# Performance work log

Measured on AMD Instinct MI355X. Metric: run time of the kernel, lower is better.

## Reference

```python
import jax, jax.numpy as jnp
import numpy as np

V = 1000   # vocab_size
E = 1024   # encoder_output_dim
D = 512    # decoder_hidden_dim
A = 512    # attention_hidden_dim
T = 128    # token_embedding_size
B = 128    # batch
P = 196    # num_pix (14x14)
L = 257    # latex length -> 256 decode steps


def setup_inputs() -> dict:
    key = jax.random.key(0)
    ks = jax.random.split(key, 16)
    def p(k, shape, scale=0.05):
        return (jax.random.normal(k, shape, jnp.float32) * scale)
    return dict(
        features=jax.random.normal(ks[0], (B, P, E), jnp.float32),
        latexes=jax.random.randint(ks[1], (B, L), 0, V),
        emb=p(ks[2], (V, T)),
        Wenc=p(ks[3], (A, E)), benc=jnp.zeros((A,), jnp.float32),
        Wdec=p(ks[4], (A, D)), bdec=jnp.zeros((A,), jnp.float32),
        Wattn=p(ks[5], (1, A)), battn=jnp.zeros((1,), jnp.float32),
        W1ih=p(ks[6], (4 * D, E + T)), W1hh=p(ks[7], (4 * D, D)),
        b1ih=jnp.zeros((4 * D,), jnp.float32), b1hh=jnp.zeros((4 * D,), jnp.float32),
        W2ih=p(ks[8], (4 * D, D)), W2hh=p(ks[9], (4 * D, D)),
        b2ih=jnp.zeros((4 * D,), jnp.float32), b2hh=jnp.zeros((4 * D,), jnp.float32),
        Wh0=p(ks[10], (D, E)), bh0=jnp.zeros((D,), jnp.float32),
        Wc0=p(ks[11], (D, E)), bc0=jnp.zeros((D,), jnp.float32),
        Wg=p(ks[12], (E, D)), bg=jnp.zeros((E,), jnp.float32),
        Wf=p(ks[13], (V, D)), bf=jnp.zeros((V,), jnp.float32),
    )


def _lstm_cell(x, h, c, Wih, Whh, bih, bhh):
    # torch.nn.LSTMCell: gates order i, f, g, o
    g = x @ Wih.T + bih + h @ Whh.T + bhh
    i, f, gg, o = jnp.split(g, 4, axis=1)
    c_new = jax.nn.sigmoid(f) * c + jax.nn.sigmoid(i) * jnp.tanh(gg)
    h_new = jax.nn.sigmoid(o) * jnp.tanh(c_new)
    return h_new, c_new


def reference(features, latexes, emb, Wenc, benc, Wdec, bdec, Wattn, battn,
              W1ih, W1hh, b1ih, b1hh, W2ih, W2hh, b2ih, b2hh,
              Wh0, bh0, Wc0, bc0, Wg, bg, Wf, bf):
    seq_length = latexes.shape[1] - 1
    embeds = emb[latexes]                      # [B, L, T]
    mean_enc = features.mean(axis=1)           # [B, E]
    h1 = mean_enc @ Wh0.T + bh0
    c1 = mean_enc @ Wc0.T + bc0
    h2, c2 = h1, c1
    # encoder branch of attention is step-invariant; hoist out of the loop
    enc_t = features @ Wenc.T + benc           # [B, P, A]
    wa = Wattn[0]                              # [A]
    ba = battn[0]

    def step(carry, emb_s):
        h1, c1, h2, c2 = carry
        dec_t = h2 @ Wdec.T + bdec                         # [B, A]
        attn = jnp.tanh(enc_t + dec_t[:, None, :]) @ wa + ba  # [B, P]
        alpha = jax.nn.softmax(attn, axis=1)
        awe = jnp.einsum('bp,bpe->be', alpha, features)    # [B, E]
        x1 = jnp.concatenate([emb_s, awe], axis=1)         # [B, T+E]
        # NOTE: original computes gate = sigmoid(Wg h2 + bg) and multiplies the
        # attention encoding AFTER lstm1_input was built -> dead code; omitted.
        h1n, c1n = _lstm_cell(x1, h1, c1, W1ih, W1hh, b1ih, b1hh)
        h2n, c2n = _lstm_cell(h1n, h2, c2, W2ih, W2hh, b2ih, b2hh)
        out = h2n @ Wf.T + bf                              # [B, V]
        return (h1n, c1n, h2n, c2n), (out, alpha)

    emb_seq = jnp.swapaxes(embeds[:, :seq_length], 0, 1)   # [S, B, T]
    _, (preds, alphas) = jax.lax.scan(step, (h1, c1, h2, c2), emb_seq)
    preds = jnp.swapaxes(preds, 0, 1)                      # [B, S, V]
    alphas = jnp.swapaxes(alphas, 0, 1)                    # [B, S, P]
    return preds, alphas
```

## Files before the change

### kernel.cpp

```cpp
#include <hip/hip_runtime.h>
#include <stdint.h>

#define VV 1000
#define EE 1024
#define DD 512
#define AA 512
#define TT 128
#define BB 128
#define PP 196
#define SS 256

typedef unsigned short ushort_t;
typedef unsigned long long ull_t;
typedef __attribute__((ext_vector_type(8))) short short8;
typedef __attribute__((ext_vector_type(4))) float floatx4;
typedef __attribute__((ext_vector_type(4))) unsigned short ushort4_t;
typedef __attribute__((ext_vector_type(8))) unsigned short ushort8_t;
typedef __attribute__((ext_vector_type(2))) unsigned long long ull2;

__device__ __forceinline__ float bf2f(unsigned short h) {
    return __uint_as_float(((unsigned int)h) << 16);
}
__device__ __forceinline__ unsigned short f2bf(float x) {
    unsigned int u = __float_as_uint(x);
    unsigned int r = (u + 0x7fffu + ((u >> 16) & 1u)) >> 16;
    return (unsigned short)r;
}
__device__ __forceinline__ float fast_rcp(float x) { return __builtin_amdgcn_rcpf(x); }
__device__ __forceinline__ float sigmoidf_(float x) { return fast_rcp(1.f + __expf(-x)); }
__device__ __forceinline__ float tanhf_(float x) {
    float e = __expf(2.f * x);
    return 1.f - 2.f * fast_rcp(e + 1.f);
}

__device__ __forceinline__ short8 ldA16(const ushort_t* p) {
    ull2 v;
    v.x = __hip_atomic_load((const ull_t*)p, __ATOMIC_RELAXED, __HIP_MEMORY_SCOPE_AGENT);
    v.y = __hip_atomic_load((const ull_t*)p + 1, __ATOMIC_RELAXED, __HIP_MEMORY_SCOPE_AGENT);
    return __builtin_bit_cast(short8, v);
}
__device__ __forceinline__ ull_t ldA8(const ushort_t* p) {
    return __hip_atomic_load((const ull_t*)p, __ATOMIC_RELAXED, __HIP_MEMORY_SCOPE_AGENT);
}
__device__ __forceinline__ void stC8(ushort_t* p, ull_t v) {
    __hip_atomic_store((ull_t*)p, v, __ATOMIC_RELAXED, __HIP_MEMORY_SCOPE_AGENT);
}
__device__ __forceinline__ void stC4(ushort_t* p, unsigned int v) {
    __hip_atomic_store((unsigned int*)p, v, __ATOMIC_RELAXED, __HIP_MEMORY_SCOPE_AGENT);
}
__device__ __forceinline__ void stCi(int* p, int v) {
    __hip_atomic_store(p, v, __ATOMIC_RELAXED, __HIP_MEMORY_SCOPE_AGENT);
}
__device__ __forceinline__ int ld_cp(const int* p) {
    int v;
    asm volatile("global_load_dword %0, %1, off sc0 sc1\n\ts_waitcnt vmcnt(0)"
                 : "=v"(v)
                 : "v"(p)
                 : "memory");
    return v;
}

template <int NK, int CH>
__device__ __forceinline__ void gemm2_sc1(const ushort_t* __restrict__ ap,
                                          const ushort_t* __restrict__ bp0,
                                          const ushort_t* __restrict__ bp1,
                                          floatx4& acc0, floatx4& acc1) {
    static_assert(NK % CH == 0, "");
    constexpr int NCH = NK / CH;
    short8 ab[2][CH];
#pragma unroll
    for (int i = 0; i < CH; ++i) ab[0][i] = ldA16(ap + i * 32);
#pragma unroll
    for (int c = 0; c < NCH; ++c) {
        if (c + 1 < NCH) {
#pragma unroll
            for (int i = 0; i < CH; ++i)
                ab[(c + 1) & 1][i] = ldA16(ap + ((c + 1) * CH + i) * 32);
        }
#pragma unroll
        for (int i = 0; i < CH; ++i) {
            const int ks = c * CH + i;
            short8 b0 = *(const short8*)(bp0 + ks * 32);
            short8 b1 = *(const short8*)(bp1 + ks * 32);
            acc0 = __builtin_amdgcn_mfma_f32_16x16x32_bf16(ab[c & 1][i], b0, acc0, 0, 0, 0);
            acc1 = __builtin_amdgcn_mfma_f32_16x16x32_bf16(ab[c & 1][i], b1, acc1, 0, 0, 0);
        }
    }
}


__global__ void cvt_kernel(const float* __restrict__ src, ushort_t* __restrict__ dst, int n) {
    int i = blockIdx.x * 256 + threadIdx.x;
    if (i < n) dst[i] = f2bf(src[i]);
}

__global__ void zero_kernel(int* __restrict__ p, int n) {
    int i = blockIdx.x * 256 + threadIdx.x;
    if (i < n) p[i] = 0;
}

__global__ void addv_kernel(const float* __restrict__ a, const float* __restrict__ b,
                            float* __restrict__ o, int n) {
    int i = blockIdx.x * 256 + threadIdx.x;
    if (i < n) o[i] = a[i] + b[i];
}

__global__ void mean_kernel(const float* __restrict__ feat, float* __restrict__ meanv) {
    int idx = blockIdx.x * 256 + threadIdx.x;
    int b = idx >> 10;
    int e = idx & 1023;
    const float* p = feat + (size_t)b * PP * 1024 + e;
    float s = 0.f;
    for (int pp = 0; pp < PP; ++pp) s += p[(size_t)pp * 1024];
    meanv[idx] = s * (1.f / 196.f);
}

__global__ __launch_bounds__(256) void init_kernel(
    const float* __restrict__ meanv, const float* __restrict__ Wh0, const float* __restrict__ bh0,
    const float* __restrict__ Wc0, const float* __restrict__ bc0,
    float* __restrict__ c1, float* __restrict__ c2,
    ushort_t* __restrict__ h1b, ushort_t* __restrict__ h2b) {
    int b = blockIdx.x, t = threadIdx.x;
    __shared__ float ml[1024];
    for (int i = t; i < 1024; i += 256) ml[i] = meanv[b * 1024 + i];
    __syncthreads();
    for (int d = t; d < 512; d += 256) {
        const float4* wh = (const float4*)(Wh0 + (size_t)d * 1024);
        const float4* wc = (const float4*)(Wc0 + (size_t)d * 1024);
        float ah = bh0[d], ac = bc0[d];
        #pragma unroll 4
        for (int j = 0; j < 256; ++j) {
            float4 w = wh[j];
            ah += w.x * ml[4 * j] + w.y * ml[4 * j + 1] + w.z * ml[4 * j + 2] + w.w * ml[4 * j + 3];
        }
        #pragma unroll 4
        for (int j = 0; j < 256; ++j) {
            float4 w = wc[j];
            ac += w.x * ml[4 * j] + w.y * ml[4 * j + 1] + w.z * ml[4 * j + 2] + w.w * ml[4 * j + 3];
        }
        c1[b * 512 + d] = ac;
        c2[b * 512 + d] = ac;
        ushort_t hb = f2bf(ah);
        h1b[b * 512 + d] = hb;
        h2b[b * 512 + d] = hb;
    }
}

__global__ __launch_bounds__(256) void enc_gemm(
    const ushort_t* __restrict__ feat_bf, const ushort_t* __restrict__ wenc_bf,
    const float* __restrict__ benc, ushort_t* __restrict__ enc_bf) {
    const int t = threadIdx.x, blk = blockIdx.x;
    const int bm = (blk % 392) * 64, bn = (blk / 392) * 64;
    const int lane = t & 63, wv = t >> 6;
    const int n = lane & 15, q = lane >> 4;
    const int arow = bm + wv * 16 + n;
    const short8* ap = (const short8*)(feat_bf + (size_t)arow * 1024 + q * 8);
    const short8* bp0 = (const short8*)(wenc_bf + (size_t)(bn + 0 * 16 + n) * 1024 + q * 8);
    const short8* bp1 = (const short8*)(wenc_bf + (size_t)(bn + 1 * 16 + n) * 1024 + q * 8);
    const short8* bp2 = (const short8*)(wenc_bf + (size_t)(bn + 2 * 16 + n) * 1024 + q * 8);
    const short8* bp3 = (const short8*)(wenc_bf + (size_t)(bn + 3 * 16 + n) * 1024 + q * 8);
    floatx4 acc0 = {0.f, 0.f, 0.f, 0.f}, acc1 = acc0, acc2 = acc0, acc3 = acc0;
    for (int ks = 0; ks < 32; ++ks) {
        short8 a8 = ap[ks * 4];
        acc0 = __builtin_amdgcn_mfma_f32_16x16x32_bf16(a8, bp0[ks * 4], acc0, 0, 0, 0);
        acc1 = __builtin_amdgcn_mfma_f32_16x16x32_bf16(a8, bp1[ks * 4], acc1, 0, 0, 0);
        acc2 = __builtin_amdgcn_mfma_f32_16x16x32_bf16(a8, bp2[ks * 4], acc2, 0, 0, 0);
        acc3 = __builtin_amdgcn_mfma_f32_16x16x32_bf16(a8, bp3[ks * 4], acc3, 0, 0, 0);
    }
    #pragma unroll
    for (int r = 0; r < 4; ++r) {
        int m = bm + wv * 16 + q * 4 + r;
        int a0 = bn + n;
        enc_bf[(size_t)m * 512 + a0] = f2bf(acc0[r] + benc[a0]);
        enc_bf[(size_t)m * 512 + a0 + 16] = f2bf(acc1[r] + benc[a0 + 16]);
        enc_bf[(size_t)m * 512 + a0 + 32] = f2bf(acc2[r] + benc[a0 + 32]);
        enc_bf[(size_t)m * 512 + a0 + 48] = f2bf(acc3[r] + benc[a0 + 48]);
    }
}

__device__ __forceinline__ void gbar(int* __restrict__ bar, int k) {
    asm volatile("s_waitcnt vmcnt(0)" ::: "memory");
    __syncthreads();
    if (threadIdx.x == 0) {
        if (ld_cp(bar + 384) == 0) {
            const int g = blockIdx.x >> 5;
            int old = __hip_atomic_fetch_add(bar + g * 16, 1, __ATOMIC_RELAXED,
                                             __HIP_MEMORY_SCOPE_AGENT);
            const bool leader = (old + 1 == 32 * k);
            int* flag;
            if (leader) {
                int r = __hip_atomic_fetch_add(bar + 160, 1, __ATOMIC_RELAXED,
                                               __HIP_MEMORY_SCOPE_AGENT);
                if (r + 1 == 8 * k) stCi(bar + 192, k);
                flag = bar + 192;
            } else {
                flag = bar + 256 + g * 16;
            }
            int spins = 0;
            while (ld_cp(flag) < k) {
                __builtin_amdgcn_s_sleep(2);
                if (((++spins) & 255) == 0) {
                    if (ld_cp(bar + 384) != 0) break;
                    if (spins > 60000) {
                        stCi(bar + 384, 1);
                        break;
                    }
                }
            }
            if (leader) stCi(bar + 256 + g * 16, k);
        }
    }
    __syncthreads();
}

__device__ __forceinline__ void preds_tile(int w2, int s, const ushort_t* __restrict__ h2cur,
                                           const ushort_t* __restrict__ wf_bf,
                                           const float* __restrict__ bfv,
                                           float* __restrict__ out, int wv, int n, int q) {
    const int vt = w2 >> 1, mt = w2 & 1;
    const int v0 = vt * 32;
    const int m0 = mt * 64 + wv * 16;
    const int vr0 = v0 + n, vr1 = v0 + 16 + n;
    const int vc0 = vr0 < VV ? vr0 : VV - 1;
    const int vc1 = vr1 < VV ? vr1 : VV - 1;
    floatx4 acc0 = {0.f, 0.f, 0.f, 0.f}, acc1 = acc0;
    gemm2_sc1<16, 8>(h2cur + (size_t)(m0 + n) * 512 + q * 8,
                     wf_bf + (size_t)vc0 * 512 + q * 8,
                     wf_bf + (size_t)vc1 * 512 + q * 8, acc0, acc1);
    const size_t so = (size_t)(s - 1) * 1000;
    #pragma unroll
    for (int r = 0; r < 4; ++r) {
        int br = m0 + q * 4 + r;
        if (vr0 < VV) out[(size_t)br * 256000 + so + vr0] = acc0[r] + bfv[vr0];
        if (vr1 < VV) out[(size_t)br * 256000 + so + vr1] = acc1[r] + bfv[vr1];
    }
}

template <int NK1, int CH1>
__device__ __forceinline__ void lstm_phase(
    int wg, int t, int wv, int n, int q, int K1,
    const ushort_t* __restrict__ A1, const ushort_t* __restrict__ W1,
    const ushort_t* __restrict__ A2v, const ushort_t* __restrict__ W2,
    const float* __restrict__ bsum,
    float& cA, float& cB, ushort_t* __restrict__ hout, float (*glds)[65]) {
    const int mt = wg >> 5, ct = wg & 31, d0 = ct * 16;
    const int rh2 = wv & 1, ch = wv >> 1;
    const int m0 = mt * 32 + rh2 * 16;
    const int g0 = ch * 2, g1 = g0 + 1;
    floatx4 acc0 = {0.f, 0.f, 0.f, 0.f}, acc1 = acc0;
    gemm2_sc1<NK1, CH1>(A1 + (size_t)(m0 + n) * K1 + q * 8,
                        W1 + (size_t)(g0 * 512 + d0 + n) * K1 + q * 8,
                        W1 + (size_t)(g1 * 512 + d0 + n) * K1 + q * 8, acc0, acc1);
    gemm2_sc1<16, 8>(A2v + (size_t)(m0 + n) * 512 + q * 8,
                     W2 + (size_t)(g0 * 512 + d0 + n) * 512 + q * 8,
                     W2 + (size_t)(g1 * 512 + d0 + n) * 512 + q * 8, acc0, acc1);
    #pragma unroll
    for (int r = 0; r < 4; ++r) {
        glds[rh2 * 16 + q * 4 + r][g0 * 16 + n] = acc0[r];
        glds[rh2 * 16 + q * 4 + r][g1 * 16 + n] = acc1[r];
    }
    __syncthreads();
    const int bl = t >> 3, dj = (t & 7) * 2;
    const int b = mt * 32 + bl, d = d0 + dj;
    float gi0 = glds[bl][dj] + bsum[d];
    float gi1 = glds[bl][dj + 1] + bsum[d + 1];
    float gf0 = glds[bl][16 + dj] + bsum[512 + d];
    float gf1 = glds[bl][17 + dj] + bsum[512 + d + 1];
    float gg0 = glds[bl][32 + dj] + bsum[1024 + d];
    float gg1 = glds[bl][33 + dj] + bsum[1024 + d + 1];
    float go0 = glds[bl][48 + dj] + bsum[1536 + d];
    float go1 = glds[bl][49 + dj] + bsum[1536 + d + 1];
    float cn0 = sigmoidf_(gf0) * cA + sigmoidf_(gi0) * tanhf_(gg0);
    float cn1 = sigmoidf_(gf1) * cB + sigmoidf_(gi1) * tanhf_(gg1);
    cA = cn0;
    cB = cn1;
    float hn0 = sigmoidf_(go0) * tanhf_(cn0);
    float hn1 = sigmoidf_(go1) * tanhf_(cn1);
    unsigned int pk = (unsigned int)f2bf(hn0) | ((unsigned int)f2bf(hn1) << 16);
    stC4(hout + (size_t)b * 512 + d, pk);
}

__global__ __launch_bounds__(256, 1) void decode_loop(
    const ushort_t* __restrict__ enc_bf, const ushort_t* __restrict__ feat_bf,
    const ushort_t* __restrict__ wdec_bf, const ushort_t* __restrict__ wf_bf,
    const ushort_t* __restrict__ emb_bf,
    const ushort_t* __restrict__ w1ih_bf, const ushort_t* __restrict__ w1hh_bf,
    const ushort_t* __restrict__ w2ih_bf, const ushort_t* __restrict__ w2hh_bf,
    const int* __restrict__ latexes,
    const float* __restrict__ wattn, const float* __restrict__ battn,
    const float* __restrict__ bdec, const float* __restrict__ bfv,
    const float* __restrict__ b1s, const float* __restrict__ b2s,
    const float* __restrict__ c1i, const float* __restrict__ c2i,
    ushort_t* __restrict__ h1b0, ushort_t* __restrict__ h1b1,
    ushort_t* __restrict__ h2b0, ushort_t* __restrict__ h2b1,
    ushort_t* __restrict__ x1_bf,
    float* __restrict__ out, int* __restrict__ bar) {
    const int wg = blockIdx.x, t = threadIdx.x;
    const int lane = t & 63, wv = t >> 6;
    const int n = lane & 15, q = lane >> 4;

    __shared__ float wa_lds[512];
    __shared__ float h2f[512];
    __shared__ float dec_lds[512];
    __shared__ float red[256];
    __shared__ float attn_lds[200];
    __shared__ float alpha_lds[200];
    __shared__ float glds[32][65];
    __shared__ int pflag;

    float c1A = 0.f, c1B = 0.f, c2A = 0.f, c2B = 0.f;
    if (wg < 128) {
        const int mt = wg >> 5, ct = wg & 31;
        const int b = mt * 32 + (t >> 3), d = ct * 16 + (t & 7) * 2;
        c1A = c1i[b * 512 + d];
        c1B = c1i[b * 512 + d + 1];
        c2A = c2i[b * 512 + d];
        c2B = c2i[b * 512 + d + 1];
        for (int i = t; i < 512; i += 256) wa_lds[i] = wattn[i];
    }

    int bc = 0;
    for (int s = 0;; ++s) {
        const ushort_t* h1cur = (s & 1) ? h1b1 : h1b0;
        const ushort_t* h2cur = (s & 1) ? h2b1 : h2b0;
        ushort_t* h1nxt = (s & 1) ? h1b0 : h1b1;
        ushort_t* h2nxt = (s & 1) ? h2b0 : h2b1;

        if (s == SS) {
            if (wg >= 128 && wg < 192) preds_tile(wg - 128, SS, h2cur, wf_bf, bfv, out, wv, n, q);
            break;
        }
        if (threadIdx.x == 0) pflag = ld_cp(bar + 384);
        __syncthreads();
        if (pflag != 0) break;

        if (wg < BB) {
            const int b = wg;
            if (t < 32) {
                int tok = latexes[b * 257 + s];
                ull_t v = *(const ull_t*)(emb_bf + (size_t)tok * TT + t * 4);
                stC8(x1_bf + (size_t)b * 1152 + t * 4, v);
            }
            if (t < 128) {
                ull_t v = ldA8(h2cur + (size_t)b * 512 + t * 4);
                ushort4_t u = __builtin_bit_cast(ushort4_t, v);
                h2f[t * 4 + 0] = bf2f(u[0]);
                h2f[t * 4 + 1] = bf2f(u[1]);
                h2f[t * 4 + 2] = bf2f(u[2]);
                h2f[t * 4 + 3] = bf2f(u[3]);
            }
            __syncthreads();
            for (int d = t; d < 512; d += 256) {
                const ushort8_t* wr = (const ushort8_t*)(wdec_bf + (size_t)d * 512);
                float acc = 0.f;
                #pragma unroll 4
                for (int j = 0; j < 64; ++j) {
                    ushort8_t w8 = wr[j];
                    const float* h8 = &h2f[j * 8];
                    #pragma unroll
                    for (int u = 0; u < 8; ++u) acc += bf2f(w8[u]) * h8[u];
                }
                dec_lds[d] = acc + bdec[d];
            }
            __syncthreads();
            const float ba = battn[0];
            for (int p = wv; p < PP; p += 4) {
                const ushort8_t ev =
                    *(const ushort8_t*)(enc_bf + ((size_t)(b * PP + p)) * 512 + lane * 8);
                float acc = 0.f;
                #pragma unroll
                for (int u = 0; u < 8; ++u) {
                    float x = bf2f(ev[u]) + dec_lds[lane * 8 + u];
                    acc += wa_lds[lane * 8 + u] * tanhf_(x);
                }
                #pragma unroll
                for (int off = 32; off > 0; off >>= 1) acc += __shfl_xor(acc, off, 64);
                if (lane == 0) attn_lds[p] = acc + ba;
            }
            __syncthreads();
            float logit = (t < PP) ? attn_lds[t] : -1e30f;
            red[t] = logit;
            __syncthreads();
            for (int st = 128; st > 0; st >>= 1) {
                if (t < st) red[t] = fmaxf(red[t], red[t + st]);
                __syncthreads();
            }
            float mx = red[0];
            __syncthreads();
            float e = (t < PP) ? __expf(logit - mx) : 0.f;
            red[t] = e;
            __syncthreads();
            for (int st = 128; st > 0; st >>= 1) {
                if (t < st) red[t] += red[t + st];
                __syncthreads();
            }
            float inv = fast_rcp(red[0]);
            float a = e * inv;
            if (t < PP) {
                alpha_lds[t] = a;
                out[(size_t)32768000 + (size_t)b * 50176 + (size_t)s * 196 + t] = a;
            }
            __syncthreads();
            float a0 = 0.f, a1 = 0.f, a2 = 0.f, a3 = 0.f;
            const int e0 = t * 4;
            #pragma unroll 4
            for (int p = 0; p < PP; ++p) {
                float av = alpha_lds[p];
                ushort4_t f4 = *(const ushort4_t*)(feat_bf + ((size_t)(b * PP + p)) * 1024 + e0);
                a0 += av * bf2f(f4[0]);
                a1 += av * bf2f(f4[1]);
                a2 += av * bf2f(f4[2]);
                a3 += av * bf2f(f4[3]);
            }
            ull_t pk = (ull_t)f2bf(a0) | ((ull_t)f2bf(a1) << 16) |
                       ((ull_t)f2bf(a2) << 32) | ((ull_t)f2bf(a3) << 48);
            stC8(x1_bf + (size_t)b * 1152 + TT + e0, pk);
        } else if (wg < 192 && s > 0) {
            preds_tile(wg - 128, s, h2cur, wf_bf, bfv, out, wv, n, q);
        }
        gbar(bar, ++bc);

        if (wg < 128)
            lstm_phase<36, 9>(wg, t, wv, n, q, 1152, x1_bf, w1ih_bf, h1cur, w1hh_bf,
                              b1s, c1A, c1B, h1nxt, glds);
        gbar(bar, ++bc);

        if (wg < 128)
            lstm_phase<16, 8>(wg, t, wv, n, q, 512, h1nxt, w2ih_bf, h2cur, w2hh_bf,
                              b2s, c2A, c2B, h2nxt, glds);
        gbar(bar, ++bc);
    }
}

extern "C" void kernel_launch(void* const* d_in, const int* in_sizes, int n_in,
                              void* d_out, int out_size, void* d_ws, size_t ws_size,
                              hipStream_t stream) {
    const float* features = (const float*)d_in[0];
    const int* latexes = (const int*)d_in[1];
    const float* emb = (const float*)d_in[2];
    const float* Wenc = (const float*)d_in[3];
    const float* benc = (const float*)d_in[4];
    const float* Wdec = (const float*)d_in[5];
    const float* bdec = (const float*)d_in[6];
    const float* Wattn = (const float*)d_in[7];
    const float* battn = (const float*)d_in[8];
    const float* W1ih = (const float*)d_in[9];
    const float* W1hh = (const float*)d_in[10];
    const float* b1ih = (const float*)d_in[11];
    const float* b1hh = (const float*)d_in[12];
    const float* W2ih = (const float*)d_in[13];
    const float* W2hh = (const float*)d_in[14];
    const float* b2ih = (const float*)d_in[15];
    const float* b2hh = (const float*)d_in[16];
    const float* Wh0 = (const float*)d_in[17];
    const float* bh0 = (const float*)d_in[18];
    const float* Wc0 = (const float*)d_in[19];
    const float* bc0 = (const float*)d_in[20];
    const float* Wf = (const float*)d_in[23];
    const float* bfv = (const float*)d_in[24];
    float* out = (float*)d_out;

    char* ws = (char*)d_ws;
    size_t off = 0;
    auto alloc = [&](size_t bytes) {
        void* p = ws + off;
        off += (bytes + 255) & ~(size_t)255;
        return p;
    };
    ushort_t* feat_bf = (ushort_t*)alloc(25690112ull * 2);
    ushort_t* enc_bf = (ushort_t*)alloc(12845056ull * 2);
    ushort_t* w1ih_bf = (ushort_t*)alloc(2359296ull * 2);
    ushort_t* w1hh_bf = (ushort_t*)alloc(1048576ull * 2);
    ushort_t* w2ih_bf = (ushort_t*)alloc(1048576ull * 2);
    ushort_t* w2hh_bf = (ushort_t*)alloc(1048576ull * 2);
    ushort_t* wf_bf = (ushort_t*)alloc(512000ull * 2);
    ushort_t* wdec_bf = (ushort_t*)alloc(262144ull * 2);
    ushort_t* wenc_bf = (ushort_t*)alloc(524288ull * 2);
    ushort_t* emb_bf = (ushort_t*)alloc(128000ull * 2);
    float* meanv = (float*)alloc(131072ull * 4);
    float* c1 = (float*)alloc(65536ull * 4);
    float* c2 = (float*)alloc(65536ull * 4);
    ushort_t* h1b0 = (ushort_t*)alloc(65536ull * 2);
    ushort_t* h1b1 = (ushort_t*)alloc(65536ull * 2);
    ushort_t* h2b0 = (ushort_t*)alloc(65536ull * 2);
    ushort_t* h2b1 = (ushort_t*)alloc(65536ull * 2);
    ushort_t* x1_bf = (ushort_t*)alloc(147456ull * 2);
    float* b1s = (float*)alloc(2048ull * 4);
    float* b2s = (float*)alloc(2048ull * 4);
    int* bar = (int*)alloc(512 * sizeof(int));

    auto cv = [&](const float* s, ushort_t* d, int n) {
        cvt_kernel<<<(n + 255) / 256, 256, 0, stream>>>(s, d, n);
    };
    cv(features, feat_bf, 25690112);
    cv(Wenc, wenc_bf, 524288);
    cv(W1ih, w1ih_bf, 2359296);
    cv(W1hh, w1hh_bf, 1048576);
    cv(W2ih, w2ih_bf, 1048576);
    cv(W2hh, w2hh_bf, 1048576);
    cv(Wf, wf_bf, 512000);
    cv(Wdec, wdec_bf, 262144);
    cv(emb, emb_bf, 128000);
    zero_kernel<<<2, 256, 0, stream>>>(bar, 512);
    addv_kernel<<<8, 256, 0, stream>>>(b1ih, b1hh, b1s, 2048);
    addv_kernel<<<8, 256, 0, stream>>>(b2ih, b2hh, b2s, 2048);
    mean_kernel<<<512, 256, 0, stream>>>(features, meanv);
    init_kernel<<<128, 256, 0, stream>>>(meanv, Wh0, bh0, Wc0, bc0, c1, c2, h1b0, h2b0);
    enc_gemm<<<3136, 256, 0, stream>>>(feat_bf, wenc_bf, benc, enc_bf);

    decode_loop<<<256, 256, 0, stream>>>(
        enc_bf, feat_bf, wdec_bf, wf_bf, emb_bf, w1ih_bf, w1hh_bf, w2ih_bf, w2hh_bf,
        latexes, Wattn, battn, bdec, bfv, b1s, b2s, c1, c2,
        h1b0, h1b1, h2b0, h2b1, x1_bf, out, bar);
}
```

Before: 33.89 ms.

## Split attention and context work across all 256 workgroups, move preds into LSTM1 phase

The attention logits and the context-vector reduction were computed by only 128 workgroups while the other 128 sat mostly idle. Now every workgroup takes half of the pixels for the logits and half of the encoder dimension for the weighted feature sum, with register-prefetched loads. The partial logits go through a global buffer and an extra grid barrier. The output projection is retiled to 16-wide vocab tiles across 128 workgroups and runs alongside the LSTM1 phase. The cost is one more grid-wide barrier per decode step, and each workgroup now recomputes the softmax redundantly.

```diff
diff --git a/kernel.cpp b/kernel.cpp
--- a/kernel.cpp
+++ b/kernel.cpp
@@ -51,6 +51,12 @@
 __device__ __forceinline__ void stCi(int* p, int v) {
     __hip_atomic_store(p, v, __ATOMIC_RELAXED, __HIP_MEMORY_SCOPE_AGENT);
 }
+__device__ __forceinline__ void stCf(float* p, float v) {
+    __hip_atomic_store(p, v, __ATOMIC_RELAXED, __HIP_MEMORY_SCOPE_AGENT);
+}
+__device__ __forceinline__ float ldCf(const float* p) {
+    return __hip_atomic_load(p, __ATOMIC_RELAXED, __HIP_MEMORY_SCOPE_AGENT);
+}
 __device__ __forceinline__ int ld_cp(const int* p) {
     int v;
     asm volatile("global_load_dword %0, %1, off sc0 sc1\n\ts_waitcnt vmcnt(0)"
@@ -84,6 +90,29 @@
             short8 b1 = *(const short8*)(bp1 + ks * 32);
             acc0 = __builtin_amdgcn_mfma_f32_16x16x32_bf16(ab[c & 1][i], b0, acc0, 0, 0, 0);
             acc1 = __builtin_amdgcn_mfma_f32_16x16x32_bf16(ab[c & 1][i], b1, acc1, 0, 0, 0);
+        }
+    }
+}
+
+template <int NK, int CH>
+__device__ __forceinline__ void gemm1_sc1(const ushort_t* __restrict__ ap,
+                                          const ushort_t* __restrict__ bp, floatx4& acc) {
+    static_assert(NK % CH == 0, "");
+    constexpr int NCH = NK / CH;
+    short8 ab[2][CH];
+#pragma unroll
+    for (int i = 0; i < CH; ++i) ab[0][i] = ldA16(ap + i * 32);
+#pragma unroll
+    for (int c = 0; c < NCH; ++c) {
+        if (c + 1 < NCH) {
+#pragma unroll
+            for (int i = 0; i < CH; ++i)
+                ab[(c + 1) & 1][i] = ldA16(ap + ((c + 1) * CH + i) * 32);
+        }
+#pragma unroll
+        for (int i = 0; i < CH; ++i) {
+            short8 b0 = *(const short8*)(bp + (c * CH + i) * 32);
+            acc = __builtin_amdgcn_mfma_f32_16x16x32_bf16(ab[c & 1][i], b0, acc, 0, 0, 0);
         }
     }
 }
@@ -218,21 +247,19 @@
                                            const float* __restrict__ bfv,
                                            float* __restrict__ out, int wv, int n, int q) {
     const int vt = w2 >> 1, mt = w2 & 1;
-    const int v0 = vt * 32;
+    const int v0 = vt * 16;
     const int m0 = mt * 64 + wv * 16;
-    const int vr0 = v0 + n, vr1 = v0 + 16 + n;
-    const int vc0 = vr0 < VV ? vr0 : VV - 1;
-    const int vc1 = vr1 < VV ? vr1 : VV - 1;
-    floatx4 acc0 = {0.f, 0.f, 0.f, 0.f}, acc1 = acc0;
-    gemm2_sc1<16, 8>(h2cur + (size_t)(m0 + n) * 512 + q * 8,
-                     wf_bf + (size_t)vc0 * 512 + q * 8,
-                     wf_bf + (size_t)vc1 * 512 + q * 8, acc0, acc1);
-    const size_t so = (size_t)(s - 1) * 1000;
-    #pragma unroll
-    for (int r = 0; r < 4; ++r) {
-        int br = m0 + q * 4 + r;
-        if (vr0 < VV) out[(size_t)br * 256000 + so + vr0] = acc0[r] + bfv[vr0];
-        if (vr1 < VV) out[(size_t)br * 256000 + so + vr1] = acc1[r] + bfv[vr1];
+    const int vr = v0 + n;
+    const int vc = vr < VV ? vr : VV - 1;
+    floatx4 acc = {0.f, 0.f, 0.f, 0.f};
+    gemm1_sc1<16, 8>(h2cur + (size_t)(m0 + n) * 512 + q * 8,
+                     wf_bf + (size_t)vc * 512 + q * 8, acc);
+    if (vr < VV) {
+        const float cb = bfv[vr];
+        const size_t so = (size_t)(s - 1) * 1000 + vr;
+        #pragma unroll
+        for (int r = 0; r < 4; ++r)
+            out[(size_t)(m0 + q * 4 + r) * 256000 + so] = acc[r] + cb;
     }
 }
 
@@ -293,7 +320,7 @@
     const float* __restrict__ c1i, const float* __restrict__ c2i,
     ushort_t* __restrict__ h1b0, ushort_t* __restrict__ h1b1,
     ushort_t* __restrict__ h2b0, ushort_t* __restrict__ h2b1,
-    ushort_t* __restrict__ x1_bf,
+    ushort_t* __restrict__ x1_bf, float* __restrict__ logit_g,
     float* __restrict__ out, int* __restrict__ bar) {
     const int wg = blockIdx.x, t = threadIdx.x;
     const int lane = t & 63, wv = t >> 6;
@@ -316,8 +343,8 @@
         c1B = c1i[b * 512 + d + 1];
         c2A = c2i[b * 512 + d];
         c2B = c2i[b * 512 + d + 1];
-        for (int i = t; i < 512; i += 256) wa_lds[i] = wattn[i];
-    }
+    }
+    for (int i = t; i < 512; i += 256) wa_lds[i] = wattn[i];
 
     int bc = 0;
     for (int s = 0;; ++s) {
@@ -327,16 +354,17 @@
         ushort_t* h2nxt = (s & 1) ? h2b0 : h2b1;
 
         if (s == SS) {
-            if (wg >= 128 && wg < 192) preds_tile(wg - 128, SS, h2cur, wf_bf, bfv, out, wv, n, q);
+            if (wg >= 128) preds_tile(wg - 128, SS, h2cur, wf_bf, bfv, out, wv, n, q);
             break;
         }
         if (threadIdx.x == 0) pflag = ld_cp(bar + 384);
         __syncthreads();
         if (pflag != 0) break;
 
-        if (wg < BB) {
-            const int b = wg;
-            if (t < 32) {
+        {
+            const int b = wg & 127, ph = wg >> 7;
+            const int pbase = ph * 98;
+            if (ph == 0 && t < 32) {
                 int tok = latexes[b * 257 + s];
                 ull_t v = *(const ull_t*)(emb_bf + (size_t)tok * TT + t * 4);
                 stC8(x1_bf + (size_t)b * 1152 + t * 4, v);
@@ -364,19 +392,50 @@
             }
             __syncthreads();
             const float ba = battn[0];
-            for (int p = wv; p < PP; p += 4) {
-                const ushort8_t ev =
-                    *(const ushort8_t*)(enc_bf + ((size_t)(b * PP + p)) * 512 + lane * 8);
-                float acc = 0.f;
-                #pragma unroll
-                for (int u = 0; u < 8; ++u) {
-                    float x = bf2f(ev[u]) + dec_lds[lane * 8 + u];
-                    acc += wa_lds[lane * 8 + u] * tanhf_(x);
+            float wl[8], dl[8];
+            #pragma unroll
+            for (int u = 0; u < 8; ++u) {
+                wl[u] = wa_lds[lane * 8 + u];
+                dl[u] = dec_lds[lane * 8 + u];
+            }
+            const ushort_t* eb = enc_bf + ((size_t)(b * PP + pbase)) * 512 + lane * 8;
+            ushort8_t ev[2][5];
+            #pragma unroll
+            for (int i = 0; i < 5; ++i) {
+                int idx = wv + i * 4;
+                if (idx > 97) idx = 97;
+                ev[0][i] = *(const ushort8_t*)(eb + (size_t)idx * 512);
+            }
+            #pragma unroll
+            for (int blk = 0; blk < 5; ++blk) {
+                if (blk + 1 < 5) {
+                    #pragma unroll
+                    for (int i = 0; i < 5; ++i) {
+                        int idx = wv + ((blk + 1) * 5 + i) * 4;
+                        if (idx > 97) idx = 97;
+                        ev[(blk + 1) & 1][i] = *(const ushort8_t*)(eb + (size_t)idx * 512);
+                    }
                 }
                 #pragma unroll
-                for (int off = 32; off > 0; off >>= 1) acc += __shfl_xor(acc, off, 64);
-                if (lane == 0) attn_lds[p] = acc + ba;
-            }
+                for (int i = 0; i < 5; ++i) {
+                    int idx = wv + (blk * 5 + i) * 4;
+                    if (idx > 97) idx = 97;
+                    ushort8_t e8 = ev[blk & 1][i];
+                    float acc = 0.f;
+                    #pragma unroll
+                    for (int u = 0; u < 8; ++u)
+                        acc += wl[u] * tanhf_(bf2f(e8[u]) + dl[u]);
+                    #pragma unroll
+                    for (int off = 32; off > 0; off >>= 1) acc += __shfl_xor(acc, off, 64);
+                    if (lane == 0) stCf(logit_g + b * 256 + pbase + idx, acc + ba);
+                }
+            }
+        }
+        gbar(bar, ++bc);
+
+        {
+            const int b = wg & 127, eh = wg >> 7;
+            if (t < PP) attn_lds[t] = ldCf(logit_g + b * 256 + t);
             __syncthreads();
             float logit = (t < PP) ? attn_lds[t] : -1e30f;
             red[t] = logit;
@@ -398,31 +457,44 @@
             float a = e * inv;
             if (t < PP) {
                 alpha_lds[t] = a;
-                out[(size_t)32768000 + (size_t)b * 50176 + (size_t)s * 196 + t] = a;
-            }
-            __syncthreads();
-            float a0 = 0.f, a1 = 0.f, a2 = 0.f, a3 = 0.f;
-            const int e0 = t * 4;
-            #pragma unroll 4
-            for (int p = 0; p < PP; ++p) {
-                float av = alpha_lds[p];
-                ushort4_t f4 = *(const ushort4_t*)(feat_bf + ((size_t)(b * PP + p)) * 1024 + e0);
-                a0 += av * bf2f(f4[0]);
-                a1 += av * bf2f(f4[1]);
-                a2 += av * bf2f(f4[2]);
-                a3 += av * bf2f(f4[3]);
-            }
-            ull_t pk = (ull_t)f2bf(a0) | ((ull_t)f2bf(a1) << 16) |
-                       ((ull_t)f2bf(a2) << 32) | ((ull_t)f2bf(a3) << 48);
-            stC8(x1_bf + (size_t)b * 1152 + TT + e0, pk);
-        } else if (wg < 192 && s > 0) {
-            preds_tile(wg - 128, s, h2cur, wf_bf, bfv, out, wv, n, q);
+                if (eh == 0)
+                    out[(size_t)32768000 + (size_t)b * 50176 + (size_t)s * 196 + t] = a;
+            }
+            __syncthreads();
+            const int e0 = eh * 512 + t * 2;
+            const ushort_t* fb = feat_bf + (size_t)b * PP * 1024 + e0;
+            float a0 = 0.f, a1 = 0.f;
+            unsigned int st2[2][28];
+            #pragma unroll
+            for (int i = 0; i < 28; ++i)
+                st2[0][i] = *(const unsigned int*)(fb + (size_t)i * 1024);
+            #pragma unroll
+            for (int blk = 0; blk < 7; ++blk) {
+                if (blk + 1 < 7) {
+                    #pragma unroll
+                    for (int i = 0; i < 28; ++i)
+                        st2[(blk + 1) & 1][i] =
+                            *(const unsigned int*)(fb + (size_t)((blk + 1) * 28 + i) * 1024);
+                }
+                #pragma unroll
+                for (int i = 0; i < 28; ++i) {
+                    float av = alpha_lds[blk * 28 + i];
+                    unsigned int fv = st2[blk & 1][i];
+                    a0 += av * bf2f((unsigned short)(fv & 0xffffu));
+                    a1 += av * bf2f((unsigned short)(fv >> 16));
+                }
+            }
+            unsigned int pk = (unsigned int)f2bf(a0) | ((unsigned int)f2bf(a1) << 16);
+            stC4(x1_bf + (size_t)b * 1152 + TT + e0, pk);
         }
         gbar(bar, ++bc);
 
-        if (wg < 128)
+        if (wg < 128) {
             lstm_phase<36, 9>(wg, t, wv, n, q, 1152, x1_bf, w1ih_bf, h1cur, w1hh_bf,
                               b1s, c1A, c1B, h1nxt, glds);
+        } else if (s > 0) {
+            preds_tile(wg - 128, s, h2cur, wf_bf, bfv, out, wv, n, q);
+        }
         gbar(bar, ++bc);
 
         if (wg < 128)
@@ -485,6 +557,7 @@
     ushort_t* h2b0 = (ushort_t*)alloc(65536ull * 2);
     ushort_t* h2b1 = (ushort_t*)alloc(65536ull * 2);
     ushort_t* x1_bf = (ushort_t*)alloc(147456ull * 2);
+    float* logit_g = (float*)alloc(32768ull * 4);
     float* b1s = (float*)alloc(2048ull * 4);
     float* b2s = (float*)alloc(2048ull * 4);
     int* bar = (int*)alloc(512 * sizeof(int));
@@ -511,5 +584,5 @@
     decode_loop<<<256, 256, 0, stream>>>(
         enc_bf, feat_bf, wdec_bf, wf_bf, emb_bf, w1ih_bf, w1hh_bf, w2ih_bf, w2hh_bf,
         latexes, Wattn, battn, bdec, bfv, b1s, b2s, c1, c2,
-        h1b0, h1b1, h2b0, h2b1, x1_bf, out, bar);
-}
+        h1b0, h1b1, h2b0, h2b1, x1_bf, logit_g, out, bar);
+}
```

Result: slower. 42.58 ms (+25.7%).
